# Optimization experiments

Hardware: AMD Instinct MI355X
Metric: run time of the kernel (lower is better)

## Reference

```python
import jax, jax.numpy as jnp
import numpy as np

B, H, OH, C, T = 512, 1024, 4096, 512, 40


def setup_inputs() -> dict:
    key = jax.random.key(0)
    ks = jax.random.split(key, 5)
    scaled = lambda k, sh, fan: (jax.random.normal(k, sh, jnp.float32) / np.sqrt(fan).astype(np.float32))
    return dict(
        z=jax.random.normal(ks[0], (B, H), jnp.float32),
        timestamps=jnp.arange(T, dtype=jnp.float32) * 0.1,  # spacing == rk4 step_size
        W1=scaled(ks[1], (H, OH), H), b1=jnp.zeros((OH,), jnp.float32),
        W2=scaled(ks[2], (OH, H), OH), b2=jnp.zeros((H,), jnp.float32),
        Wf=scaled(ks[3], (H, C), H), bf=jnp.zeros((C,), jnp.float32),
    )


def reference(z, timestamps, W1, b1, W2, b2, Wf, bf):
    # odefunc: autonomous neural-ODE MLP f(y) = tanh(y W1 + b1) W2 + b2
    def f(y):
        return jnp.tanh(y @ W1 + b1) @ W2 + b2

    # torchdiffeq 'rk4' = 3/8-rule RK4 (rk4_alt_step_func); one step per
    # timestamp interval since spacing == step_size == 0.1
    def step(y, ts):
        t0, t1 = ts
        dt = t1 - t0
        k1 = f(y)
        k2 = f(y + dt * k1 / 3.0)
        k3 = f(y + dt * (k2 - k1 / 3.0))
        k4 = f(y + dt * (k1 - k2 + k3))
        y_new = y + dt * (k1 + 3.0 * (k2 + k3) + k4) / 8.0
        return y_new, y_new

    _, ys = jax.lax.scan(step, z, (timestamps[:-1], timestamps[1:]))
    pred_z = jnp.concatenate([z[None], ys], axis=0)  # [T, B, H], includes y0
    return jax.nn.softmax(pred_z @ Wf + bf, axis=-1)  # [T, B, C]
```

## Files before the change

kernel.cpp:

```cpp
#include <hip/hip_runtime.h>
#include <hip/hip_bf16.h>
#include <math.h>

using bf16 = __hip_bfloat16;
typedef __bf16 bf16x8 __attribute__((ext_vector_type(8)));
typedef float f32x4 __attribute__((ext_vector_type(4)));

static constexpr int NB = 512, NH = 1024, NOH = 4096, NC = 512, NT = 40;
static constexpr int SPLITK = 4;


__global__ void transpose_cast(const float* __restrict__ W, bf16* __restrict__ WT,
                               int K, int N) {
  __shared__ float tile[32][33];
  const int n0 = blockIdx.x * 32;
  const int k0 = blockIdx.y * 32;
  const int tx = threadIdx.x;
  const int ty = threadIdx.y;
#pragma unroll
  for (int i = 0; i < 4; ++i) {
    int r = ty + i * 8;
    tile[r][tx] = W[(size_t)(k0 + r) * N + n0 + tx];
  }
  __syncthreads();
#pragma unroll
  for (int i = 0; i < 4; ++i) {
    int r = ty + i * 8;
    const int n = n0 + r, k = k0 + tx;
    WT[(size_t)n * K + (k ^ ((n & 7) << 3))] = __float2bfloat16(tile[tx][r]);
  }
}

__global__ void init_state(const float* __restrict__ z, float* __restrict__ y,
                           bf16* __restrict__ yb, bf16* __restrict__ pred0) {
  const int i = blockIdx.x * 256 + threadIdx.x;
  const int r = i >> 10, c = i & (NH - 1);
  float v = z[i];
  y[i] = v;
  bf16 b = __float2bfloat16(v);
  const int sw = r * NH + (c ^ ((r & 7) << 3));
  yb[sw] = b;
  pred0[sw] = b;
}

template <int EPI>
__global__ __launch_bounds__(256, 2) void gemm_stage(
    const bf16* __restrict__ A, const bf16* __restrict__ BT,
    const float* __restrict__ bias, bf16* __restrict__ outB,
    float* __restrict__ outF) {
  constexpr int BK = 64;
  constexpr int KCH = 1024;
  constexpr int KST = (EPI == 0) ? NH : NOH;
  constexpr int NOUT = (EPI == 0) ? NOH : NH;
  constexpr int NI = KCH / BK;

  __shared__ __align__(16) bf16 As[4][64 * BK];
  __shared__ __align__(16) bf16 Bs[4][64 * BK];

  const int tid = threadIdx.x;
  const int lane = tid & 63;
  const int wave = tid >> 6;
  const int wr = wave >> 1, wc = wave & 1;
  const int l15 = lane & 15, kg = lane >> 4;
  const int xorB = (l15 & 7) << 4;
  const int srow = tid >> 3;
  const int scol = (tid & 7) * 8;

  const int bid = blockIdx.x;
  const int xcd = bid & 7, slot = bid >> 3;
  int row0, col0, kbeg;
  float* outFb = outF;
  if constexpr (EPI == 0) {
    col0 = (xcd + ((slot & 7) << 3)) * 64;
    row0 = (slot >> 3) * 64;
    kbeg = 0;
  } else {
    col0 = (xcd + ((slot & 1) << 3)) * 64;
    const int kz = (slot >> 1) & 3;
    row0 = (slot >> 3) * 64;
    kbeg = kz * KCH;
    outFb = outF + (size_t)kz * (NB * NH);
  }

  f32x4 acc[2][2] = {};

  auto stage = [&](int buf, int kt) {
#pragma unroll
    for (int i = 0; i < 2; ++i) {
      const bf16* ga = A + (size_t)(row0 + i * 32 + srow) * KST + kt + scol;
      __builtin_amdgcn_global_load_lds(
          (const __attribute__((address_space(1))) void*)ga,
          (__attribute__((address_space(3))) void*)&As[buf][i * 2048 + tid * 8],
          16, 0, 0);
      const bf16* gb = BT + (size_t)(col0 + i * 32 + srow) * KST + kt + scol;
      __builtin_amdgcn_global_load_lds(
          (const __attribute__((address_space(1))) void*)gb,
          (__attribute__((address_space(3))) void*)&Bs[buf][i * 2048 + tid * 8],
          16, 0, 0);
    }
  };

  stage(0, kbeg);
  stage(1, kbeg + BK);
  stage(2, kbeg + 2 * BK);

#pragma unroll 1
  for (int j = 0; j < NI; ++j) {
    if (j < NI - 2)       asm volatile("s_waitcnt vmcnt(8)" ::: "memory");
    else if (j == NI - 2) asm volatile("s_waitcnt vmcnt(4)" ::: "memory");
    else                  asm volatile("s_waitcnt vmcnt(0)" ::: "memory");
    __builtin_amdgcn_s_barrier();
    __builtin_amdgcn_sched_barrier(0);
    if (j + 3 < NI) stage((j + 3) & 3, kbeg + (j + 3) * BK);

    const char* Ab = (const char*)&As[j & 3][0];
    const char* Bb = (const char*)&Bs[j & 3][0];
#pragma unroll
    for (int ks = 0; ks < BK; ks += 32) {
      const int kb2 = (ks + kg * 8) * 2;
      bf16x8 af[2], bf_[2];
#pragma unroll
      for (int mi = 0; mi < 2; ++mi) {
        const int r = wr * 32 + mi * 16 + l15;
        af[mi] = *reinterpret_cast<const bf16x8*>(Ab + ((r * 128 + kb2) ^ xorB));
      }
#pragma unroll
      for (int ni = 0; ni < 2; ++ni) {
        const int r = wc * 32 + ni * 16 + l15;
        bf_[ni] = *reinterpret_cast<const bf16x8*>(Bb + ((r * 128 + kb2) ^ xorB));
      }
#pragma unroll
      for (int mi = 0; mi < 2; ++mi)
#pragma unroll
        for (int ni = 0; ni < 2; ++ni)
          acc[mi][ni] = __builtin_amdgcn_mfma_f32_16x16x32_bf16(
              af[mi], bf_[ni], acc[mi][ni], 0, 0, 0);
    }
  }

#pragma unroll
  for (int mi = 0; mi < 2; ++mi) {
    const int gr0 = row0 + wr * 32 + mi * 16 + kg * 4;
#pragma unroll
    for (int ni = 0; ni < 2; ++ni) {
      const int gcol = col0 + wc * 32 + ni * 16 + l15;
      float b = 0.0f;
      if constexpr (EPI == 0) b = bias[gcol];
#pragma unroll
      for (int j = 0; j < 4; ++j) {
        const int r = gr0 + j;
        if constexpr (EPI == 0) {
          outB[(size_t)r * NOUT + (gcol ^ ((r & 7) << 3))] =
              __float2bfloat16(tanhf(acc[mi][ni][j] + b));
        } else {
          outFb[(size_t)r * NOUT + gcol] = acc[mi][ni][j];
        }
      }
    }
  }
}

__global__ void combine_stage(const float* __restrict__ part,
                              const float* __restrict__ b2,
                              float* __restrict__ y, bf16* __restrict__ yb,
                              float* __restrict__ k1, float* __restrict__ k2,
                              float* __restrict__ k3, bf16* __restrict__ pred_next,
                              const float* __restrict__ ts, int t, int s) {
  const int i = blockIdx.x * 256 + threadIdx.x;
  const float dt = ts[t + 1] - ts[t];
  constexpr int NE = NB * NH;

  f32x4 sum = {};
#pragma unroll
  for (int z = 0; z < SPLITK; ++z)
    sum += *reinterpret_cast<const f32x4*>(part + (size_t)z * NE + (size_t)i * 4);

  const int col = (i * 4) & (NH - 1);
  const int row = (i * 4) >> 10;
  const f32x4 bb = *reinterpret_cast<const f32x4*>(b2 + col);
  const f32x4 ksv = sum + bb;
  const f32x4 yv = *reinterpret_cast<const f32x4*>(y + (size_t)i * 4);

  f32x4 ynext;
  if (s == 1) {
    *reinterpret_cast<f32x4*>(k1 + (size_t)i * 4) = ksv;
    ynext = yv + ksv * (dt / 3.0f);
  } else if (s == 2) {
    const f32x4 k1v = *reinterpret_cast<const f32x4*>(k1 + (size_t)i * 4);
    *reinterpret_cast<f32x4*>(k2 + (size_t)i * 4) = ksv;
    ynext = yv + (ksv - k1v * (1.0f / 3.0f)) * dt;
  } else if (s == 3) {
    const f32x4 k1v = *reinterpret_cast<const f32x4*>(k1 + (size_t)i * 4);
    const f32x4 k2v = *reinterpret_cast<const f32x4*>(k2 + (size_t)i * 4);
    *reinterpret_cast<f32x4*>(k3 + (size_t)i * 4) = ksv;
    ynext = yv + (k1v - k2v + ksv) * dt;
  } else {
    const f32x4 k1v = *reinterpret_cast<const f32x4*>(k1 + (size_t)i * 4);
    const f32x4 k2v = *reinterpret_cast<const f32x4*>(k2 + (size_t)i * 4);
    const f32x4 k3v = *reinterpret_cast<const f32x4*>(k3 + (size_t)i * 4);
    ynext = yv + (k1v + (k2v + k3v) * 3.0f + ksv) * (dt * 0.125f);
    *reinterpret_cast<f32x4*>(y + (size_t)i * 4) = ynext;
  }

  union { bf16 h[4]; unsigned long long u; } pk;
#pragma unroll
  for (int j = 0; j < 4; ++j) pk.h[j] = __float2bfloat16(ynext[j]);
  const size_t sw = (size_t)row * NH + (col ^ ((row & 7) << 3));
  *reinterpret_cast<unsigned long long*>(yb + sw) = pk.u;
  if (s == 4) *reinterpret_cast<unsigned long long*>(pred_next + sw) = pk.u;
}

__global__ __launch_bounds__(256, 1) void proj_gemm(
    const bf16* __restrict__ A, const bf16* __restrict__ BT,
    int M, int N, int K, const float* __restrict__ bias,
    float* __restrict__ outF) {
  __shared__ __align__(16) bf16 As[2][128 * 64];
  __shared__ __align__(16) bf16 Bs[2][128 * 64];

  const int tid = threadIdx.x;
  const int lane = tid & 63;
  const int wave = tid >> 6;
  const int wr = wave >> 1, wc = wave & 1;
  const int row0 = blockIdx.y * 128, col0 = blockIdx.x * 128;
  const int l15 = lane & 15, kg = lane >> 4;
  const int xorB = (l15 & 7) << 4;
  const int srow = tid >> 3;
  const int scol = (tid & 7) * 8;

  f32x4 acc[4][4] = {};

  auto stage = [&](int buf, int kt) {
#pragma unroll
    for (int i = 0; i < 4; ++i) {
      const bf16* ga = A + (size_t)(row0 + i * 32 + srow) * K + kt + scol;
      __builtin_amdgcn_global_load_lds(
          (const __attribute__((address_space(1))) void*)ga,
          (__attribute__((address_space(3))) void*)&As[buf][i * 2048 + tid * 8],
          16, 0, 0);
      const bf16* gb = BT + (size_t)(col0 + i * 32 + srow) * K + kt + scol;
      __builtin_amdgcn_global_load_lds(
          (const __attribute__((address_space(1))) void*)gb,
          (__attribute__((address_space(3))) void*)&Bs[buf][i * 2048 + tid * 8],
          16, 0, 0);
    }
  };

  stage(0, 0);
  __syncthreads();
  int cur = 0;

  for (int kt = 0; kt < K; kt += 64) {
    if (kt + 64 < K) stage(cur ^ 1, kt + 64);
#pragma unroll
    for (int ks = 0; ks < 64; ks += 32) {
      const int kb2 = (ks + kg * 8) * 2;
      bf16x8 af[4], bf_[4];
#pragma unroll
      for (int mi = 0; mi < 4; ++mi) {
        const int r = wr * 64 + mi * 16 + l15;
        af[mi] = *reinterpret_cast<const bf16x8*>(
            (const char*)&As[cur][0] + ((r * 128 + kb2) ^ xorB));
      }
#pragma unroll
      for (int ni = 0; ni < 4; ++ni) {
        const int r = wc * 64 + ni * 16 + l15;
        bf_[ni] = *reinterpret_cast<const bf16x8*>(
            (const char*)&Bs[cur][0] + ((r * 128 + kb2) ^ xorB));
      }
#pragma unroll
      for (int mi = 0; mi < 4; ++mi)
#pragma unroll
        for (int ni = 0; ni < 4; ++ni)
          acc[mi][ni] = __builtin_amdgcn_mfma_f32_16x16x32_bf16(
              af[mi], bf_[ni], acc[mi][ni], 0, 0, 0);
    }
    __syncthreads();
    cur ^= 1;
  }

#pragma unroll
  for (int mi = 0; mi < 4; ++mi) {
    const int gr0 = row0 + wr * 64 + mi * 16 + kg * 4;
#pragma unroll
    for (int ni = 0; ni < 4; ++ni) {
      const int gcol = col0 + wc * 64 + ni * 16 + l15;
      const float b = bias[gcol];
#pragma unroll
      for (int j = 0; j < 4; ++j)
        outF[(size_t)(gr0 + j) * N + gcol] = acc[mi][ni][j] + b;
    }
  }
}

__global__ void softmax_rows(float* __restrict__ out) {
  const int row = blockIdx.x * 4 + (threadIdx.x >> 6);
  const int lane = threadIdx.x & 63;
  float* p = out + (size_t)row * NC + lane * 8;
  f32x4 a = *reinterpret_cast<const f32x4*>(p);
  f32x4 b = *reinterpret_cast<const f32x4*>(p + 4);

  float m = fmaxf(fmaxf(fmaxf(a[0], a[1]), fmaxf(a[2], a[3])),
                  fmaxf(fmaxf(b[0], b[1]), fmaxf(b[2], b[3])));
#pragma unroll
  for (int off = 32; off > 0; off >>= 1) m = fmaxf(m, __shfl_xor(m, off));

  f32x4 ea, eb;
  float sum = 0.0f;
#pragma unroll
  for (int j = 0; j < 4; ++j) { ea[j] = expf(a[j] - m); sum += ea[j]; }
#pragma unroll
  for (int j = 0; j < 4; ++j) { eb[j] = expf(b[j] - m); sum += eb[j]; }
#pragma unroll
  for (int off = 32; off > 0; off >>= 1) sum += __shfl_xor(sum, off);

  const float inv = 1.0f / sum;
  ea *= inv;
  eb *= inv;
  *reinterpret_cast<f32x4*>(p) = ea;
  *reinterpret_cast<f32x4*>(p + 4) = eb;
}

extern "C" void kernel_launch(void* const* d_in, const int* in_sizes, int n_in,
                              void* d_out, int out_size, void* d_ws, size_t ws_size,
                              hipStream_t stream) {
  const float* z = (const float*)d_in[0];
  const float* ts = (const float*)d_in[1];
  const float* W1 = (const float*)d_in[2];
  const float* b1 = (const float*)d_in[3];
  const float* W2 = (const float*)d_in[4];
  const float* b2 = (const float*)d_in[5];
  const float* Wf = (const float*)d_in[6];
  const float* bfv = (const float*)d_in[7];

  char* w = (char*)d_ws;
  bf16* W1bT = (bf16*)w;          w += (size_t)NOH * NH * 2;
  bf16* W2bT = (bf16*)w;          w += (size_t)NH * NOH * 2;
  bf16* WfT  = (bf16*)w;          w += (size_t)NC * NH * 2;
  float* y   = (float*)w;         w += (size_t)NB * NH * 4;
  bf16* yb   = (bf16*)w;          w += (size_t)NB * NH * 2;
  float* k1  = (float*)w;         w += (size_t)NB * NH * 4;
  float* k2  = (float*)w;         w += (size_t)NB * NH * 4;
  float* k3  = (float*)w;         w += (size_t)NB * NH * 4;
  bf16* h    = (bf16*)w;          w += (size_t)NB * NOH * 2;
  float* part = (float*)w;        w += (size_t)SPLITK * NB * NH * 4;
  bf16* pred = (bf16*)w;          w += (size_t)NT * NB * NH * 2;

  float* logits = (float*)d_out;

  transpose_cast<<<dim3(NOH / 32, NH / 32), dim3(32, 8), 0, stream>>>(W1, W1bT, NH, NOH);
  transpose_cast<<<dim3(NH / 32, NOH / 32), dim3(32, 8), 0, stream>>>(W2, W2bT, NOH, NH);
  transpose_cast<<<dim3(NC / 32, NH / 32), dim3(32, 8), 0, stream>>>(Wf, WfT, NH, NC);
  init_state<<<(NB * NH) / 256, 256, 0, stream>>>(z, y, yb, pred);

  for (int t = 0; t < NT - 1; ++t) {
    for (int s = 1; s <= 4; ++s) {
      gemm_stage<0><<<512, 256, 0, stream>>>(yb, W1bT, b1, h, nullptr);
      gemm_stage<1><<<512, 256, 0, stream>>>(h, W2bT, nullptr, nullptr, part);
      combine_stage<<<512, 256, 0, stream>>>(
          part, b2, y, yb, k1, k2, k3, pred + (size_t)(t + 1) * NB * NH, ts, t, s);
    }
  }

  proj_gemm<<<dim3(NC / 128, (NT * NB) / 128), 256, 0, stream>>>(
      pred, WfT, NT * NB, NC, NH, bfv, logits);
  softmax_rows<<<(NT * NB) / 4, 256, 0, stream>>>(logits);
}
```

Baseline: 4.922 ms.

## Fuse split-K reduction and RK4 combine into second GEMM via atomic counters

Removes the separate combine kernel. The last split-K block to finish each output tile, detected with a per-tile atomic arrival counter, sums the partials and applies the RK4 stage update. The GEMM pipeline also drops from 4 to 3 LDS buffers with prefetch depth 2 and raises launch bounds to 3 blocks per CU for occupancy. This saves one launch and one full pass over the partials per stage, at the cost of serialised tail work and atomic memory-ordering subtleties.

```diff
diff --git a/kernel.cpp b/kernel.cpp
--- a/kernel.cpp
+++ b/kernel.cpp
@@ -8,6 +8,18 @@
 
 static constexpr int NB = 512, NH = 1024, NOH = 4096, NC = 512, NT = 40;
 static constexpr int SPLITK = 4;
+static constexpr int NCNT = 128;
+
+#define AL(p) __hip_atomic_load((p), __ATOMIC_RELAXED, __HIP_MEMORY_SCOPE_AGENT)
+#define ASF(p, v) __hip_atomic_store((p), (v), __ATOMIC_RELAXED, __HIP_MEMORY_SCOPE_AGENT)
+#define AFA(p, v) __hip_atomic_fetch_add((p), (v), __ATOMIC_RELAXED, __HIP_MEMORY_SCOPE_AGENT)
+
+__device__ __forceinline__ float lo32f(unsigned long long v) {
+  return __uint_as_float((unsigned)v);
+}
+__device__ __forceinline__ float hi32f(unsigned long long v) {
+  return __uint_as_float((unsigned)(v >> 32));
+}
 
 
 __global__ void transpose_cast(const float* __restrict__ W, bf16* __restrict__ WT,
@@ -32,7 +44,8 @@
 }
 
 __global__ void init_state(const float* __restrict__ z, float* __restrict__ y,
-                           bf16* __restrict__ yb, bf16* __restrict__ pred0) {
+                           bf16* __restrict__ yb, bf16* __restrict__ pred0,
+                           unsigned* __restrict__ cnt) {
   const int i = blockIdx.x * 256 + threadIdx.x;
   const int r = i >> 10, c = i & (NH - 1);
   float v = z[i];
@@ -41,21 +54,25 @@
   const int sw = r * NH + (c ^ ((r & 7) << 3));
   yb[sw] = b;
   pred0[sw] = b;
+  if (i < (NT - 1) * 4 * NCNT) cnt[i] = 0u;
 }
 
 template <int EPI>
-__global__ __launch_bounds__(256, 2) void gemm_stage(
+__global__ __launch_bounds__(256, 3) void gemm_stage(
     const bf16* __restrict__ A, const bf16* __restrict__ BT,
     const float* __restrict__ bias, bf16* __restrict__ outB,
-    float* __restrict__ outF) {
+    float* __restrict__ part, float* __restrict__ y, bf16* __restrict__ yb,
+    float* __restrict__ k1, float* __restrict__ k2, float* __restrict__ k3,
+    bf16* __restrict__ pred_next, const float* __restrict__ ts, int t, int s,
+    unsigned* __restrict__ cnt) {
   constexpr int BK = 64;
   constexpr int KCH = 1024;
   constexpr int KST = (EPI == 0) ? NH : NOH;
   constexpr int NOUT = (EPI == 0) ? NOH : NH;
   constexpr int NI = KCH / BK;
 
-  __shared__ __align__(16) bf16 As[4][64 * BK];
-  __shared__ __align__(16) bf16 Bs[4][64 * BK];
+  __shared__ __align__(16) bf16 As[3][64 * BK];
+  __shared__ __align__(16) bf16 Bs[3][64 * BK];
 
   const int tid = threadIdx.x;
   const int lane = tid & 63;
@@ -68,18 +85,18 @@
 
   const int bid = blockIdx.x;
   const int xcd = bid & 7, slot = bid >> 3;
-  int row0, col0, kbeg;
-  float* outFb = outF;
+  int row0, col0, kbeg, kz = 0, strip = 0, rb = 0;
   if constexpr (EPI == 0) {
     col0 = (xcd + ((slot & 7) << 3)) * 64;
     row0 = (slot >> 3) * 64;
     kbeg = 0;
   } else {
-    col0 = (xcd + ((slot & 1) << 3)) * 64;
-    const int kz = (slot >> 1) & 3;
-    row0 = (slot >> 3) * 64;
+    strip = xcd + ((slot & 1) << 3);
+    col0 = strip * 64;
+    kz = (slot >> 1) & 3;
+    rb = slot >> 3;
+    row0 = rb * 64;
     kbeg = kz * KCH;
-    outFb = outF + (size_t)kz * (NB * NH);
   }
 
   f32x4 acc[2][2] = {};
@@ -102,19 +119,19 @@
 
   stage(0, kbeg);
   stage(1, kbeg + BK);
-  stage(2, kbeg + 2 * BK);
+  int cur = 0, nxt = 2;
 
 #pragma unroll 1
   for (int j = 0; j < NI; ++j) {
-    if (j < NI - 2)       asm volatile("s_waitcnt vmcnt(8)" ::: "memory");
-    else if (j == NI - 2) asm volatile("s_waitcnt vmcnt(4)" ::: "memory");
-    else                  asm volatile("s_waitcnt vmcnt(0)" ::: "memory");
+    if (j < NI - 1) asm volatile("s_waitcnt vmcnt(4)" ::: "memory");
+    else            asm volatile("s_waitcnt vmcnt(0)" ::: "memory");
     __builtin_amdgcn_s_barrier();
     __builtin_amdgcn_sched_barrier(0);
-    if (j + 3 < NI) stage((j + 3) & 3, kbeg + (j + 3) * BK);
-
-    const char* Ab = (const char*)&As[j & 3][0];
-    const char* Bb = (const char*)&Bs[j & 3][0];
+    if (j + 2 < NI) stage(nxt, kbeg + (j + 2) * BK);
+    __builtin_amdgcn_sched_barrier(0);
+
+    const char* Ab = (const char*)&As[cur][0];
+    const char* Bb = (const char*)&Bs[cur][0];
 #pragma unroll
     for (int ks = 0; ks < BK; ks += 32) {
       const int kb2 = (ks + kg * 8) * 2;
@@ -136,78 +153,94 @@
           acc[mi][ni] = __builtin_amdgcn_mfma_f32_16x16x32_bf16(
               af[mi], bf_[ni], acc[mi][ni], 0, 0, 0);
     }
-  }
-
-#pragma unroll
-  for (int mi = 0; mi < 2; ++mi) {
-    const int gr0 = row0 + wr * 32 + mi * 16 + kg * 4;
-#pragma unroll
-    for (int ni = 0; ni < 2; ++ni) {
-      const int gcol = col0 + wc * 32 + ni * 16 + l15;
-      float b = 0.0f;
-      if constexpr (EPI == 0) b = bias[gcol];
-#pragma unroll
-      for (int j = 0; j < 4; ++j) {
-        const int r = gr0 + j;
-        if constexpr (EPI == 0) {
+    cur = (cur == 2) ? 0 : cur + 1;
+    nxt = (nxt == 2) ? 0 : nxt + 1;
+  }
+
+  if constexpr (EPI == 0) {
+#pragma unroll
+    for (int mi = 0; mi < 2; ++mi) {
+      const int gr0 = row0 + wr * 32 + mi * 16 + kg * 4;
+#pragma unroll
+      for (int ni = 0; ni < 2; ++ni) {
+        const int gcol = col0 + wc * 32 + ni * 16 + l15;
+        const float b = bias[gcol];
+#pragma unroll
+        for (int j = 0; j < 4; ++j) {
+          const int r = gr0 + j;
           outB[(size_t)r * NOUT + (gcol ^ ((r & 7) << 3))] =
               __float2bfloat16(tanhf(acc[mi][ni][j] + b));
+        }
+      }
+    }
+  } else {
+    float* pz = part + (size_t)kz * (NB * NH);
+#pragma unroll
+    for (int mi = 0; mi < 2; ++mi) {
+      const int gr0 = row0 + wr * 32 + mi * 16 + kg * 4;
+#pragma unroll
+      for (int ni = 0; ni < 2; ++ni) {
+        const int gcol = col0 + wc * 32 + ni * 16 + l15;
+#pragma unroll
+        for (int j = 0; j < 4; ++j)
+          ASF(&pz[(size_t)(gr0 + j) * NH + gcol], acc[mi][ni][j]);
+      }
+    }
+    __syncthreads();
+    __shared__ unsigned arrS;
+    if (tid == 0) arrS = AFA(&cnt[rb * 16 + strip], 1u);
+    __syncthreads();
+    if (arrS == (unsigned)(SPLITK - 1)) {
+      const float dtv = ts[t + 1] - ts[t];
+#pragma unroll
+      for (int q = 0; q < 4; ++q) {
+        const int v = q * 256 + tid;
+        const int r = v >> 4, c4 = v & 15;
+        const int row = row0 + r, col = col0 + c4 * 4;
+        const size_t gi = (size_t)row * NH + col;
+        f32x4 sum = {};
+#pragma unroll
+        for (int z = 0; z < SPLITK; ++z) {
+          const unsigned long long* pp =
+              (const unsigned long long*)(part + (size_t)z * (NB * NH) + gi);
+          unsigned long long u0 = AL(pp), u1 = AL(pp + 1);
+          sum[0] += lo32f(u0); sum[1] += hi32f(u0);
+          sum[2] += lo32f(u1); sum[3] += hi32f(u1);
+        }
+        const f32x4 bb = *reinterpret_cast<const f32x4*>(bias + col);
+        const f32x4 ksv = sum + bb;
+        const f32x4 yv = *reinterpret_cast<const f32x4*>(y + gi);
+        f32x4 yn;
+        if (s == 1) {
+          *reinterpret_cast<f32x4*>(k1 + gi) = ksv;
+          yn = yv + ksv * (dtv / 3.0f);
+        } else if (s == 2) {
+          const f32x4 k1v = *reinterpret_cast<const f32x4*>(k1 + gi);
+          *reinterpret_cast<f32x4*>(k2 + gi) = ksv;
+          yn = yv + (ksv - k1v * (1.0f / 3.0f)) * dtv;
+        } else if (s == 3) {
+          const f32x4 k1v = *reinterpret_cast<const f32x4*>(k1 + gi);
+          const f32x4 k2v = *reinterpret_cast<const f32x4*>(k2 + gi);
+          *reinterpret_cast<f32x4*>(k3 + gi) = ksv;
+          yn = yv + (k1v - k2v + ksv) * dtv;
         } else {
-          outFb[(size_t)r * NOUT + gcol] = acc[mi][ni][j];
+          const f32x4 k1v = *reinterpret_cast<const f32x4*>(k1 + gi);
+          const f32x4 k2v = *reinterpret_cast<const f32x4*>(k2 + gi);
+          const f32x4 k3v = *reinterpret_cast<const f32x4*>(k3 + gi);
+          yn = yv + (k1v + (k2v + k3v) * 3.0f + ksv) * (dtv * 0.125f);
+          *reinterpret_cast<f32x4*>(y + gi) = yn;
         }
-      }
-    }
-  }
-}
-
-__global__ void combine_stage(const float* __restrict__ part,
-                              const float* __restrict__ b2,
-                              float* __restrict__ y, bf16* __restrict__ yb,
-                              float* __restrict__ k1, float* __restrict__ k2,
-                              float* __restrict__ k3, bf16* __restrict__ pred_next,
-                              const float* __restrict__ ts, int t, int s) {
-  const int i = blockIdx.x * 256 + threadIdx.x;
-  const float dt = ts[t + 1] - ts[t];
-  constexpr int NE = NB * NH;
-
-  f32x4 sum = {};
-#pragma unroll
-  for (int z = 0; z < SPLITK; ++z)
-    sum += *reinterpret_cast<const f32x4*>(part + (size_t)z * NE + (size_t)i * 4);
-
-  const int col = (i * 4) & (NH - 1);
-  const int row = (i * 4) >> 10;
-  const f32x4 bb = *reinterpret_cast<const f32x4*>(b2 + col);
-  const f32x4 ksv = sum + bb;
-  const f32x4 yv = *reinterpret_cast<const f32x4*>(y + (size_t)i * 4);
-
-  f32x4 ynext;
-  if (s == 1) {
-    *reinterpret_cast<f32x4*>(k1 + (size_t)i * 4) = ksv;
-    ynext = yv + ksv * (dt / 3.0f);
-  } else if (s == 2) {
-    const f32x4 k1v = *reinterpret_cast<const f32x4*>(k1 + (size_t)i * 4);
-    *reinterpret_cast<f32x4*>(k2 + (size_t)i * 4) = ksv;
-    ynext = yv + (ksv - k1v * (1.0f / 3.0f)) * dt;
-  } else if (s == 3) {
-    const f32x4 k1v = *reinterpret_cast<const f32x4*>(k1 + (size_t)i * 4);
-    const f32x4 k2v = *reinterpret_cast<const f32x4*>(k2 + (size_t)i * 4);
-    *reinterpret_cast<f32x4*>(k3 + (size_t)i * 4) = ksv;
-    ynext = yv + (k1v - k2v + ksv) * dt;
-  } else {
-    const f32x4 k1v = *reinterpret_cast<const f32x4*>(k1 + (size_t)i * 4);
-    const f32x4 k2v = *reinterpret_cast<const f32x4*>(k2 + (size_t)i * 4);
-    const f32x4 k3v = *reinterpret_cast<const f32x4*>(k3 + (size_t)i * 4);
-    ynext = yv + (k1v + (k2v + k3v) * 3.0f + ksv) * (dt * 0.125f);
-    *reinterpret_cast<f32x4*>(y + (size_t)i * 4) = ynext;
-  }
-
-  union { bf16 h[4]; unsigned long long u; } pk;
-#pragma unroll
-  for (int j = 0; j < 4; ++j) pk.h[j] = __float2bfloat16(ynext[j]);
-  const size_t sw = (size_t)row * NH + (col ^ ((row & 7) << 3));
-  *reinterpret_cast<unsigned long long*>(yb + sw) = pk.u;
-  if (s == 4) *reinterpret_cast<unsigned long long*>(pred_next + sw) = pk.u;
+        union { bf16 h4[4]; unsigned long long u; } pk;
+#pragma unroll
+        for (int j = 0; j < 4; ++j) pk.h4[j] = __float2bfloat16(yn[j]);
+        const size_t sw =
+            (size_t)row * NH + (((col & ~7) ^ ((row & 7) << 3)) | (col & 7));
+        *reinterpret_cast<unsigned long long*>(yb + sw) = pk.u;
+        if (s == 4)
+          *reinterpret_cast<unsigned long long*>(pred_next + sw) = pk.u;
+      }
+    }
+  }
 }
 
 __global__ __launch_bounds__(256, 1) void proj_gemm(
@@ -344,20 +377,24 @@
   bf16* h    = (bf16*)w;          w += (size_t)NB * NOH * 2;
   float* part = (float*)w;        w += (size_t)SPLITK * NB * NH * 4;
   bf16* pred = (bf16*)w;          w += (size_t)NT * NB * NH * 2;
+  unsigned* cnt = (unsigned*)w;   w += (size_t)(NT - 1) * 4 * NCNT * 4;
 
   float* logits = (float*)d_out;
 
   transpose_cast<<<dim3(NOH / 32, NH / 32), dim3(32, 8), 0, stream>>>(W1, W1bT, NH, NOH);
   transpose_cast<<<dim3(NH / 32, NOH / 32), dim3(32, 8), 0, stream>>>(W2, W2bT, NOH, NH);
   transpose_cast<<<dim3(NC / 32, NH / 32), dim3(32, 8), 0, stream>>>(Wf, WfT, NH, NC);
-  init_state<<<(NB * NH) / 256, 256, 0, stream>>>(z, y, yb, pred);
+  init_state<<<(NB * NH) / 256, 256, 0, stream>>>(z, y, yb, pred, cnt);
 
   for (int t = 0; t < NT - 1; ++t) {
     for (int s = 1; s <= 4; ++s) {
-      gemm_stage<0><<<512, 256, 0, stream>>>(yb, W1bT, b1, h, nullptr);
-      gemm_stage<1><<<512, 256, 0, stream>>>(h, W2bT, nullptr, nullptr, part);
-      combine_stage<<<512, 256, 0, stream>>>(
-          part, b2, y, yb, k1, k2, k3, pred + (size_t)(t + 1) * NB * NH, ts, t, s);
+      gemm_stage<0><<<512, 256, 0, stream>>>(
+          yb, W1bT, b1, h, nullptr, nullptr, nullptr, nullptr, nullptr,
+          nullptr, nullptr, ts, t, s, nullptr);
+      gemm_stage<1><<<512, 256, 0, stream>>>(
+          h, W2bT, b2, nullptr, part, y, yb, k1, k2, k3,
+          pred + (size_t)(t + 1) * NB * NH, ts, t, s,
+          cnt + (size_t)(t * 4 + (s - 1)) * NCNT);
     }
   }
 
```

Result: slower. 5.071 ms (+3.0%).

## Cut GEMM LDS ring to three stages and reuse it for final projection

Applied to the files above, without the earlier changes.

The stage GEMM kernel's shared-memory ring buffer shrinks from four to three stages (prefetch depth two instead of three), and launch bounds rise to three blocks per CU so more workgroups can be resident. The separate 128x128-tile projection GEMM is removed, and the final logits projection now runs through a new EPI==2 variant of the same 64x64-tile kernel, with bias added in the epilogue. The goal is higher occupancy to hide latency in the many small per-step GEMMs. The cost is a shallower prefetch pipeline and possibly more register pressure, plus a smaller-tile projection GEMM with less data reuse.

```diff
diff --git a/kernel.cpp b/kernel.cpp
--- a/kernel.cpp
+++ b/kernel.cpp
@@ -44,18 +44,18 @@
 }
 
 template <int EPI>
-__global__ __launch_bounds__(256, 2) void gemm_stage(
+__global__ __launch_bounds__(256, 3) void gemm_stage(
     const bf16* __restrict__ A, const bf16* __restrict__ BT,
     const float* __restrict__ bias, bf16* __restrict__ outB,
     float* __restrict__ outF) {
   constexpr int BK = 64;
   constexpr int KCH = 1024;
-  constexpr int KST = (EPI == 0) ? NH : NOH;
-  constexpr int NOUT = (EPI == 0) ? NOH : NH;
+  constexpr int KST = (EPI == 1) ? NOH : NH;
+  constexpr int NOUT = (EPI == 0) ? NOH : (EPI == 1) ? NH : NC;
   constexpr int NI = KCH / BK;
 
-  __shared__ __align__(16) bf16 As[4][64 * BK];
-  __shared__ __align__(16) bf16 Bs[4][64 * BK];
+  __shared__ __align__(16) bf16 As[3][64 * BK];
+  __shared__ __align__(16) bf16 Bs[3][64 * BK];
 
   const int tid = threadIdx.x;
   const int lane = tid & 63;
@@ -74,12 +74,16 @@
     col0 = (xcd + ((slot & 7) << 3)) * 64;
     row0 = (slot >> 3) * 64;
     kbeg = 0;
-  } else {
+  } else if constexpr (EPI == 1) {
     col0 = (xcd + ((slot & 1) << 3)) * 64;
     const int kz = (slot >> 1) & 3;
     row0 = (slot >> 3) * 64;
     kbeg = kz * KCH;
     outFb = outF + (size_t)kz * (NB * NH);
+  } else {
+    col0 = xcd * 64;
+    row0 = slot * 64;
+    kbeg = 0;
   }
 
   f32x4 acc[2][2] = {};
@@ -102,19 +106,18 @@
 
   stage(0, kbeg);
   stage(1, kbeg + BK);
-  stage(2, kbeg + 2 * BK);
+  int cur = 0, nxt = 2;
 
 #pragma unroll 1
   for (int j = 0; j < NI; ++j) {
-    if (j < NI - 2)       asm volatile("s_waitcnt vmcnt(8)" ::: "memory");
-    else if (j == NI - 2) asm volatile("s_waitcnt vmcnt(4)" ::: "memory");
-    else                  asm volatile("s_waitcnt vmcnt(0)" ::: "memory");
+    if (j < NI - 1) asm volatile("s_waitcnt vmcnt(4)" ::: "memory");
+    else            asm volatile("s_waitcnt vmcnt(0)" ::: "memory");
     __builtin_amdgcn_s_barrier();
     __builtin_amdgcn_sched_barrier(0);
-    if (j + 3 < NI) stage((j + 3) & 3, kbeg + (j + 3) * BK);
-
-    const char* Ab = (const char*)&As[j & 3][0];
-    const char* Bb = (const char*)&Bs[j & 3][0];
+    if (j + 2 < NI) stage(nxt, kbeg + (j + 2) * BK);
+
+    const char* Ab = (const char*)&As[cur][0];
+    const char* Bb = (const char*)&Bs[cur][0];
 #pragma unroll
     for (int ks = 0; ks < BK; ks += 32) {
       const int kb2 = (ks + kg * 8) * 2;
@@ -136,6 +139,8 @@
           acc[mi][ni] = __builtin_amdgcn_mfma_f32_16x16x32_bf16(
               af[mi], bf_[ni], acc[mi][ni], 0, 0, 0);
     }
+    cur = (cur == 2) ? 0 : cur + 1;
+    nxt = (nxt == 2) ? 0 : nxt + 1;
   }
 
 #pragma unroll
@@ -145,15 +150,17 @@
     for (int ni = 0; ni < 2; ++ni) {
       const int gcol = col0 + wc * 32 + ni * 16 + l15;
       float b = 0.0f;
-      if constexpr (EPI == 0) b = bias[gcol];
+      if constexpr (EPI != 1) b = bias[gcol];
 #pragma unroll
       for (int j = 0; j < 4; ++j) {
         const int r = gr0 + j;
         if constexpr (EPI == 0) {
           outB[(size_t)r * NOUT + (gcol ^ ((r & 7) << 3))] =
               __float2bfloat16(tanhf(acc[mi][ni][j] + b));
+        } else if constexpr (EPI == 1) {
+          outFb[(size_t)r * NOUT + gcol] = acc[mi][ni][j];
         } else {
-          outFb[(size_t)r * NOUT + gcol] = acc[mi][ni][j];
+          outFb[(size_t)r * NOUT + gcol] = acc[mi][ni][j] + b;
         }
       }
     }
@@ -210,88 +217,6 @@
   if (s == 4) *reinterpret_cast<unsigned long long*>(pred_next + sw) = pk.u;
 }
 
-__global__ __launch_bounds__(256, 1) void proj_gemm(
-    const bf16* __restrict__ A, const bf16* __restrict__ BT,
-    int M, int N, int K, const float* __restrict__ bias,
-    float* __restrict__ outF) {
-  __shared__ __align__(16) bf16 As[2][128 * 64];
-  __shared__ __align__(16) bf16 Bs[2][128 * 64];
-
-  const int tid = threadIdx.x;
-  const int lane = tid & 63;
-  const int wave = tid >> 6;
-  const int wr = wave >> 1, wc = wave & 1;
-  const int row0 = blockIdx.y * 128, col0 = blockIdx.x * 128;
-  const int l15 = lane & 15, kg = lane >> 4;
-  const int xorB = (l15 & 7) << 4;
-  const int srow = tid >> 3;
-  const int scol = (tid & 7) * 8;
-
-  f32x4 acc[4][4] = {};
-
-  auto stage = [&](int buf, int kt) {
-#pragma unroll
-    for (int i = 0; i < 4; ++i) {
-      const bf16* ga = A + (size_t)(row0 + i * 32 + srow) * K + kt + scol;
-      __builtin_amdgcn_global_load_lds(
-          (const __attribute__((address_space(1))) void*)ga,
-          (__attribute__((address_space(3))) void*)&As[buf][i * 2048 + tid * 8],
-          16, 0, 0);
-      const bf16* gb = BT + (size_t)(col0 + i * 32 + srow) * K + kt + scol;
-      __builtin_amdgcn_global_load_lds(
-          (const __attribute__((address_space(1))) void*)gb,
-          (__attribute__((address_space(3))) void*)&Bs[buf][i * 2048 + tid * 8],
-          16, 0, 0);
-    }
-  };
-
-  stage(0, 0);
-  __syncthreads();
-  int cur = 0;
-
-  for (int kt = 0; kt < K; kt += 64) {
-    if (kt + 64 < K) stage(cur ^ 1, kt + 64);
-#pragma unroll
-    for (int ks = 0; ks < 64; ks += 32) {
-      const int kb2 = (ks + kg * 8) * 2;
-      bf16x8 af[4], bf_[4];
-#pragma unroll
-      for (int mi = 0; mi < 4; ++mi) {
-        const int r = wr * 64 + mi * 16 + l15;
-        af[mi] = *reinterpret_cast<const bf16x8*>(
-            (const char*)&As[cur][0] + ((r * 128 + kb2) ^ xorB));
-      }
-#pragma unroll
-      for (int ni = 0; ni < 4; ++ni) {
-        const int r = wc * 64 + ni * 16 + l15;
-        bf_[ni] = *reinterpret_cast<const bf16x8*>(
-            (const char*)&Bs[cur][0] + ((r * 128 + kb2) ^ xorB));
-      }
-#pragma unroll
-      for (int mi = 0; mi < 4; ++mi)
-#pragma unroll
-        for (int ni = 0; ni < 4; ++ni)
-          acc[mi][ni] = __builtin_amdgcn_mfma_f32_16x16x32_bf16(
-              af[mi], bf_[ni], acc[mi][ni], 0, 0, 0);
-    }
-    __syncthreads();
-    cur ^= 1;
-  }
-
-#pragma unroll
-  for (int mi = 0; mi < 4; ++mi) {
-    const int gr0 = row0 + wr * 64 + mi * 16 + kg * 4;
-#pragma unroll
-    for (int ni = 0; ni < 4; ++ni) {
-      const int gcol = col0 + wc * 64 + ni * 16 + l15;
-      const float b = bias[gcol];
-#pragma unroll
-      for (int j = 0; j < 4; ++j)
-        outF[(size_t)(gr0 + j) * N + gcol] = acc[mi][ni][j] + b;
-    }
-  }
-}
-
 __global__ void softmax_rows(float* __restrict__ out) {
   const int row = blockIdx.x * 4 + (threadIdx.x >> 6);
   const int lane = threadIdx.x & 63;
@@ -361,7 +286,6 @@
     }
   }
 
-  proj_gemm<<<dim3(NC / 128, (NT * NB) / 128), 256, 0, stream>>>(
-      pred, WfT, NT * NB, NC, NH, bfv, logits);
+  gemm_stage<2><<<2560, 256, 0, stream>>>(pred, WfT, bfv, nullptr, logits);
   softmax_rows<<<(NT * NB) / 4, 256, 0, stream>>>(logits);
 }
```

Result: no change. 4.943 ms (+0.4%).
